# Kernel tuning notes

Measured on AMD Instinct MI355X. Metric: run time of the kernel, lower is better.

Reference implementation:

```python
import jax, jax.numpy as jnp
import numpy as np

N = 262144
C = 256
G = 4096  # number of segments (upper bound on group ids)


def setup_inputs() -> dict:
    key = jax.random.key(0)
    ks = jax.random.split(key, 8)
    s = 1.0 / np.sqrt(C)
    x = jax.random.normal(ks[0], (1, N, C), dtype=jnp.float32)
    ix = jax.random.randint(ks[1], (N,), 0, G, dtype=jnp.int64)
    Wf = jax.random.uniform(ks[2], (C, C), jnp.float32, -s, s)
    bf = jax.random.uniform(ks[3], (C,), jnp.float32, -s, s)
    Wg = jax.random.uniform(ks[4], (C, C), jnp.float32, -s, s)
    bg = jax.random.uniform(ks[5], (C,), jnp.float32, -s, s)
    Wh = jax.random.uniform(ks[6], (C, C), jnp.float32, -s, s)
    bh = jax.random.uniform(ks[7], (C,), jnp.float32, -s, s)
    return {"x": x, "Wf": Wf, "bf": bf, "Wg": Wg, "bg": bg, "Wh": Wh, "bh": bh, "ix": ix}


def reference(x, Wf, bf, Wg, bg, Wh, bh, ix):
    # x: [1, N, C]; only batch 0 is used (matches torch module)
    x0 = x[0]                                    # [N, C]
    fx = x0 @ Wf.T + bf                          # [N, C]
    gx = jnp.clip(x0 @ Wg.T + bg, -50.0, 50.0)   # [N, C]
    exp_gx = jnp.exp(gx)                         # [N, C]
    # Segment softmax: sorting + cumsum group relabel in the torch code is
    # mathematically just a per-group normalized weighted sum keyed by ix.
    seg = ix.astype(jnp.int32)
    denom = jax.ops.segment_sum(exp_gx, seg, num_segments=G)   # [G, C]
    w = exp_gx / denom[seg]                                    # [N, C]
    y = jax.ops.segment_sum(fx * w, seg, num_segments=G)       # [G, C]
    y = y @ Wh.T + bh                                          # [G, C]
    out = y[seg]                                               # [N, C]
    return out[None]                                           # [1, N, C]
```

## Files before the change

### kernel.cpp

```cpp
#include <hip/hip_runtime.h>
#include <stdint.h>
#include <stddef.h>

#define N_ROWS 262144
#define CCH    256
#define NGRP   4096

typedef short bf16x8 __attribute__((ext_vector_type(8)));
typedef short bf16x4 __attribute__((ext_vector_type(4)));
typedef float f32x4  __attribute__((ext_vector_type(4)));

static __device__ __forceinline__ short f2bf(float f){
  union { float f; unsigned u; } v; v.f = f;
  unsigned u = v.u;
  unsigned r = (u + 0x7FFFu + ((u >> 16) & 1u)) >> 16;
  return (short)r;
}

typedef __attribute__((address_space(1))) const unsigned int GU32;
typedef __attribute__((address_space(3))) unsigned int LU32;
static __device__ __forceinline__ void gload_lds16(const void* g, void* l){
  __builtin_amdgcn_global_load_lds((GU32*)g, (LU32*)l, 16, 0, 0);
}

__global__ __launch_bounds__(256) void k_castw(
    const float* __restrict__ Wf, const float* __restrict__ Wg,
    const float* __restrict__ Wh,
    short* __restrict__ wfb, short* __restrict__ wgb, float* __restrict__ wht)
{
  int e = blockIdx.x * 256 + threadIdx.x;
  wfb[e] = f2bf(Wf[e]);
  wgb[e] = f2bf(Wg[e]);
  int k = e >> 8, j = e & 255;
  wht[e] = Wh[j * 256 + k];
}

__global__ __launch_bounds__(256) void k_hist(const int* __restrict__ ix, int* __restrict__ counts){
  int i = blockIdx.x * blockDim.x + threadIdx.x;
  int stride = gridDim.x * blockDim.x;
  for (; i < N_ROWS; i += stride) atomicAdd(&counts[ix[i]], 1);
}

__global__ __launch_bounds__(1024) void k_scan(const int* __restrict__ counts, int* __restrict__ cursor){
  __shared__ int sums[1024];
  int t = threadIdx.x;
  int base = t * 4;
  int c0 = counts[base], c1 = counts[base+1], c2 = counts[base+2], c3 = counts[base+3];
  sums[t] = c0 + c1 + c2 + c3;
  __syncthreads();
  for (int off = 1; off < 1024; off <<= 1){
    int v = (t >= off) ? sums[t - off] : 0;
    __syncthreads();
    sums[t] += v;
    __syncthreads();
  }
  int prev = (t == 0) ? 0 : sums[t - 1];
  cursor[base]   = prev;
  cursor[base+1] = prev + c0;
  cursor[base+2] = prev + c0 + c1;
  cursor[base+3] = prev + c0 + c1 + c2;
}

__global__ __launch_bounds__(256) void k_scatter_cast(
    const int* __restrict__ ix, int* __restrict__ cursor,
    const float* __restrict__ x, short* __restrict__ xb, int* __restrict__ gid)
{
  int wave = threadIdx.x >> 6;
  int lane = threadIdx.x & 63;
  int i = blockIdx.x * 4 + wave;
  int stride = gridDim.x * 4;
  for (; i < N_ROWS; i += stride){
    int g = ix[i];
    int p;
    if (lane == 0) p = atomicAdd(&cursor[g], 1);
    p = __shfl(p, 0);
    f32x4 v = *(const f32x4*)(x + (size_t)i * 256 + lane * 4);
    bf16x4 b;
    #pragma unroll
    for (int j = 0; j < 4; ++j) b[j] = f2bf(v[j]);
    *(bf16x4*)(xb + (size_t)p * 256 + lane * 4) = b;
    if (lane == 0) gid[p] = g;
  }
}

__global__ __launch_bounds__(512, 2) void k_gemm(
    const short* __restrict__ xb,
    const short* __restrict__ wfb, const short* __restrict__ wgb,
    const float* __restrict__ bfp, const float* __restrict__ bgp,
    const int* __restrict__ gid,
    float* __restrict__ numer, float* __restrict__ denom)
{
  __shared__ short bst[64][512];

  const int tid  = threadIdx.x;
  const int wave = tid >> 6;
  const int lane = tid & 63;
  const int l16  = lane & 15;
  const int quad = lane >> 4;

  const int p     = blockIdx.x;
  const int xcd   = p & 7;
  const int ixd   = p >> 3;
  const int cg    = ixd & 3;
  const int bslot = xcd * 16 + (ixd >> 2);
  const int j0    = cg * 64;

  #pragma unroll
  for (int q = 0; q < 8; ++q){
    int f = wave * 8 + q;
    int mat = f >> 5, ks = (f >> 2) & 7, t = f & 3;
    const short* wsrc = mat ? wgb : wfb;
    const short* src = wsrc + (size_t)(j0 + t * 16 + l16) * 256 + ks * 32 + quad * 8;
    gload_lds16(src, &bst[f][0]);
  }
  __syncthreads();

  float bfr[4], bgr[4];
  #pragma unroll
  for (int t = 0; t < 4; ++t){
    bfr[t] = bfp[j0 + t * 16 + l16];
    bgr[t] = bgp[j0 + t * 16 + l16];
  }

  for (int tile = bslot; tile < N_ROWS / 256; tile += 128){
    const int row0 = tile * 256 + wave * 32;
    const int l31  = lane & 31;
    const int gidv = gid[row0 + l31];
    const short* xr0 = xb + (size_t)(row0 + l16) * 256 + quad * 8;
    const short* xr1 = xr0 + 16 * 256;

    f32x4 accF[2][4], accG[2][4];
    #pragma unroll
    for (int rg = 0; rg < 2; ++rg)
      #pragma unroll
      for (int t = 0; t < 4; ++t){
        accF[rg][t] = (f32x4){0.f,0.f,0.f,0.f};
        accG[rg][t] = (f32x4){0.f,0.f,0.f,0.f};
      }

    #pragma unroll
    for (int kc = 0; kc < 4; ++kc){
      bf16x8 a[2][2];
      a[0][0] = *(const bf16x8*)(xr0 + kc * 64);
      a[0][1] = *(const bf16x8*)(xr0 + kc * 64 + 32);
      a[1][0] = *(const bf16x8*)(xr1 + kc * 64);
      a[1][1] = *(const bf16x8*)(xr1 + kc * 64 + 32);
      __builtin_amdgcn_s_setprio(1);
      #pragma unroll
      for (int ks = 0; ks < 2; ++ks){
        const int kk = kc * 2 + ks;
        #pragma unroll
        for (int t = 0; t < 4; ++t){
          bf16x8 bF = *(const bf16x8*)&bst[kk * 4 + t][lane * 8];
          accF[0][t] = __builtin_amdgcn_mfma_f32_16x16x32_bf16(a[0][ks], bF, accF[0][t], 0, 0, 0);
          accF[1][t] = __builtin_amdgcn_mfma_f32_16x16x32_bf16(a[1][ks], bF, accF[1][t], 0, 0, 0);
          bf16x8 bG = *(const bf16x8*)&bst[32 + kk * 4 + t][lane * 8];
          accG[0][t] = __builtin_amdgcn_mfma_f32_16x16x32_bf16(a[0][ks], bG, accG[0][t], 0, 0, 0);
          accG[1][t] = __builtin_amdgcn_mfma_f32_16x16x32_bf16(a[1][ks], bG, accG[1][t], 0, 0, 0);
        }
      }
      __builtin_amdgcn_s_setprio(0);
    }

    #pragma unroll
    for (int rg = 0; rg < 2; ++rg)
      #pragma unroll
      for (int t = 0; t < 4; ++t)
        #pragma unroll
        for (int r = 0; r < 4; ++r){
          float g = accG[rg][t][r] + bgr[t];
          g = fminf(fmaxf(g, -50.f), 50.f);
          float e = __expf(g);
          accF[rg][t][r] = (accF[rg][t][r] + bfr[t]) * e;
          accG[rg][t][r] = e;
        }

    int gprev = __shfl(gidv, (l31 + 31) & 31);
    bool head = (l31 == 0) || (gidv != gprev);
    unsigned long long hb = __ballot(head) & 0xFFFFFFFFull;
    int start = 0;
    while (start < 32){
      int g = __shfl(gidv, start);
      unsigned long long rest = (hb >> 1) >> start;
      int end = rest ? (start + 1 + __builtin_ctzll(rest)) : 32;
      #pragma unroll
      for (int t = 0; t < 4; ++t){
        float sF = 0.f, sE = 0.f;
        #pragma unroll
        for (int rg = 0; rg < 2; ++rg)
          #pragma unroll
          for (int r = 0; r < 4; ++r){
            int rl = rg * 16 + quad * 4 + r;
            bool in = (rl >= start) && (rl < end);
            sF += in ? accF[rg][t][r] : 0.f;
            sE += in ? accG[rg][t][r] : 0.f;
          }
        sF += __shfl_xor(sF, 16); sF += __shfl_xor(sF, 32);
        sE += __shfl_xor(sE, 16); sE += __shfl_xor(sE, 32);
        if (quad == 0){
          atomicAdd(&numer[(size_t)g * 256 + j0 + t * 16 + l16], sF);
          atomicAdd(&denom[(size_t)g * 256 + j0 + t * 16 + l16], sE);
        }
      }
      start = end;
    }
  }
}

__global__ __launch_bounds__(256) void k_yh(
    const float* __restrict__ numer, const float* __restrict__ denom,
    const float* __restrict__ wht, const float* __restrict__ bh,
    float* __restrict__ yh)
{
  __shared__ float ys[16][256];
  int t = threadIdx.x;
  int g0 = blockIdx.x * 16;
  #pragma unroll
  for (int gg = 0; gg < 16; ++gg){
    size_t idx = (size_t)(g0 + gg) * 256 + t;
    float d = denom[idx];
    ys[gg][t] = (d != 0.f) ? (numer[idx] / d) : 0.f;
  }
  __syncthreads();
  float acc[16];
  #pragma unroll
  for (int gg = 0; gg < 16; ++gg) acc[gg] = 0.f;
  for (int k = 0; k < 256; k += 4){
    float w0 = wht[(k+0) * 256 + t];
    float w1 = wht[(k+1) * 256 + t];
    float w2 = wht[(k+2) * 256 + t];
    float w3 = wht[(k+3) * 256 + t];
    #pragma unroll
    for (int gg = 0; gg < 16; ++gg)
      acc[gg] += w0 * ys[gg][k] + w1 * ys[gg][k+1] + w2 * ys[gg][k+2] + w3 * ys[gg][k+3];
  }
  float b = bh[t];
  #pragma unroll
  for (int gg = 0; gg < 16; ++gg) yh[(size_t)(g0 + gg) * 256 + t] = acc[gg] + b;
}

__global__ __launch_bounds__(256) void k_out(const int* __restrict__ ix,
    const float* __restrict__ yh, float* __restrict__ out)
{
  int wave = threadIdx.x >> 6;
  int lane = threadIdx.x & 63;
  int i = blockIdx.x * 4 + wave;
  int stride = gridDim.x * 4;
  for (; i < N_ROWS; i += stride){
    int g = ix[i];
    f32x4 v = *(const f32x4*)(yh + (size_t)g * 256 + lane * 4);
    *(f32x4*)(out + (size_t)i * 256 + lane * 4) = v;
  }
}

extern "C" void kernel_launch(void* const* d_in, const int* in_sizes, int n_in,
                              void* d_out, int out_size, void* d_ws, size_t ws_size,
                              hipStream_t stream)
{
  const float* x  = (const float*)d_in[0];
  const float* Wf = (const float*)d_in[1];
  const float* bf = (const float*)d_in[2];
  const float* Wg = (const float*)d_in[3];
  const float* bg = (const float*)d_in[4];
  const float* Wh = (const float*)d_in[5];
  const float* bh = (const float*)d_in[6];
  const int*   ix = (const int*)d_in[7];
  float* out = (float*)d_out;

  char* ws = (char*)d_ws;
  float* numer  = (float*)(ws + 0);
  float* denom  = (float*)(ws + 4194304);
  int*   counts = (int*)  (ws + 8388608);
  int*   cursor = (int*)  (ws + 8404992);
  float* yh     = (float*)(ws + 8421376);
  float* wht    = (float*)(ws + 12615680);
  short* wfb    = (short*)(ws + 12877824);
  short* wgb    = (short*)(ws + 13008896);
  int*   gid    = (int*)  (ws + 13139968);

  short* xb = (short*)d_out;

  hipMemsetAsync(ws, 0, 8404992, stream);

  k_castw<<<256, 256, 0, stream>>>(Wf, Wg, Wh, wfb, wgb, wht);
  k_hist<<<512, 256, 0, stream>>>(ix, counts);
  k_scan<<<1, 1024, 0, stream>>>(counts, cursor);
  k_scatter_cast<<<2048, 256, 0, stream>>>(ix, cursor, x, xb, gid);
  k_gemm<<<512, 512, 0, stream>>>(xb, wfb, wgb, bf, bg, gid, numer, denom);
  k_yh<<<256, 256, 0, stream>>>(numer, denom, wht, bh, yh);
  k_out<<<2048, 256, 0, stream>>>(ix, yh, out);
}
```

Baseline: 861.2 us.

## Switch gemm to 32x32x16 MFMA with 32-column blocks and more blocks

Rewrites the fused f/g projection kernel to use 32x32x16 bf16 MFMA tiles instead of 16x16x32, so each wave computes 32 rows by 32 output columns per matrix. Blocks shrink to 256 threads covering 32 columns (8 column groups) with half the LDS weight tile, and the grid grows to 2048 blocks. The segment-reduction epilogue is adapted to the 32x32 accumulator layout and needs only one cross-lane shuffle. The intent is fewer MFMA issues and cheaper reductions, but each x row is now reread by 8 column groups instead of 4, which doubles A-operand global traffic.

Result: faster. 794.1 us (-7.8%).

```diff
diff --git a/kernel.cpp b/kernel.cpp
--- a/kernel.cpp
+++ b/kernel.cpp
@@ -9,6 +9,7 @@
 typedef short bf16x8 __attribute__((ext_vector_type(8)));
 typedef short bf16x4 __attribute__((ext_vector_type(4)));
 typedef float f32x4  __attribute__((ext_vector_type(4)));
+typedef float f32x16 __attribute__((ext_vector_type(16)));
 
 static __device__ __forceinline__ short f2bf(float f){
   union { float f; unsigned u; } v; v.f = f;
@@ -83,97 +84,69 @@
   }
 }
 
-__global__ __launch_bounds__(512, 2) void k_gemm(
+__global__ __launch_bounds__(256) void k_gemm(
     const short* __restrict__ xb,
     const short* __restrict__ wfb, const short* __restrict__ wgb,
     const float* __restrict__ bfp, const float* __restrict__ bgp,
     const int* __restrict__ gid,
     float* __restrict__ numer, float* __restrict__ denom)
 {
-  __shared__ short bst[64][512];
+  __shared__ short bst[32][512];
 
   const int tid  = threadIdx.x;
   const int wave = tid >> 6;
   const int lane = tid & 63;
-  const int l16  = lane & 15;
-  const int quad = lane >> 4;
+  const int l31  = lane & 31;
+  const int hi   = lane >> 5;
 
   const int p     = blockIdx.x;
   const int xcd   = p & 7;
   const int ixd   = p >> 3;
-  const int cg    = ixd & 3;
-  const int bslot = xcd * 16 + (ixd >> 2);
-  const int j0    = cg * 64;
+  const int cg    = ixd & 7;
+  const int bslot = xcd * 32 + (ixd >> 3);
+  const int j0    = cg * 32;
 
   #pragma unroll
   for (int q = 0; q < 8; ++q){
     int f = wave * 8 + q;
-    int mat = f >> 5, ks = (f >> 2) & 7, t = f & 3;
+    int mat = f >> 4, ks = f & 15;
     const short* wsrc = mat ? wgb : wfb;
-    const short* src = wsrc + (size_t)(j0 + t * 16 + l16) * 256 + ks * 32 + quad * 8;
+    const short* src = wsrc + (size_t)(j0 + l31) * 256 + ks * 16 + hi * 8;
     gload_lds16(src, &bst[f][0]);
   }
   __syncthreads();
 
-  float bfr[4], bgr[4];
-  #pragma unroll
-  for (int t = 0; t < 4; ++t){
-    bfr[t] = bfp[j0 + t * 16 + l16];
-    bgr[t] = bgp[j0 + t * 16 + l16];
-  }
-
-  for (int tile = bslot; tile < N_ROWS / 256; tile += 128){
-    const int row0 = tile * 256 + wave * 32;
-    const int l31  = lane & 31;
+  const float bfv = bfp[j0 + l31];
+  const float bgv = bgp[j0 + l31];
+
+  for (int tile = bslot; tile < N_ROWS / 128; tile += 256){
+    const int row0 = tile * 128 + wave * 32;
     const int gidv = gid[row0 + l31];
-    const short* xr0 = xb + (size_t)(row0 + l16) * 256 + quad * 8;
-    const short* xr1 = xr0 + 16 * 256;
-
-    f32x4 accF[2][4], accG[2][4];
-    #pragma unroll
-    for (int rg = 0; rg < 2; ++rg)
-      #pragma unroll
-      for (int t = 0; t < 4; ++t){
-        accF[rg][t] = (f32x4){0.f,0.f,0.f,0.f};
-        accG[rg][t] = (f32x4){0.f,0.f,0.f,0.f};
-      }
-
-    #pragma unroll
-    for (int kc = 0; kc < 4; ++kc){
-      bf16x8 a[2][2];
-      a[0][0] = *(const bf16x8*)(xr0 + kc * 64);
-      a[0][1] = *(const bf16x8*)(xr0 + kc * 64 + 32);
-      a[1][0] = *(const bf16x8*)(xr1 + kc * 64);
-      a[1][1] = *(const bf16x8*)(xr1 + kc * 64 + 32);
+    const short* xr = xb + (size_t)(row0 + l31) * 256 + hi * 8;
+
+    f32x16 accF, accG;
+    #pragma unroll
+    for (int r = 0; r < 16; ++r){ accF[r] = 0.f; accG[r] = 0.f; }
+
+    #pragma unroll
+    for (int ks = 0; ks < 16; ++ks){
+      bf16x8 a  = *(const bf16x8*)(xr + ks * 16);
+      bf16x8 bF = *(const bf16x8*)&bst[ks][lane * 8];
+      bf16x8 bG = *(const bf16x8*)&bst[16 + ks][lane * 8];
       __builtin_amdgcn_s_setprio(1);
-      #pragma unroll
-      for (int ks = 0; ks < 2; ++ks){
-        const int kk = kc * 2 + ks;
-        #pragma unroll
-        for (int t = 0; t < 4; ++t){
-          bf16x8 bF = *(const bf16x8*)&bst[kk * 4 + t][lane * 8];
-          accF[0][t] = __builtin_amdgcn_mfma_f32_16x16x32_bf16(a[0][ks], bF, accF[0][t], 0, 0, 0);
-          accF[1][t] = __builtin_amdgcn_mfma_f32_16x16x32_bf16(a[1][ks], bF, accF[1][t], 0, 0, 0);
-          bf16x8 bG = *(const bf16x8*)&bst[32 + kk * 4 + t][lane * 8];
-          accG[0][t] = __builtin_amdgcn_mfma_f32_16x16x32_bf16(a[0][ks], bG, accG[0][t], 0, 0, 0);
-          accG[1][t] = __builtin_amdgcn_mfma_f32_16x16x32_bf16(a[1][ks], bG, accG[1][t], 0, 0, 0);
-        }
-      }
+      accF = __builtin_amdgcn_mfma_f32_32x32x16_bf16(a, bF, accF, 0, 0, 0);
+      accG = __builtin_amdgcn_mfma_f32_32x32x16_bf16(a, bG, accG, 0, 0, 0);
       __builtin_amdgcn_s_setprio(0);
     }
 
     #pragma unroll
-    for (int rg = 0; rg < 2; ++rg)
-      #pragma unroll
-      for (int t = 0; t < 4; ++t)
-        #pragma unroll
-        for (int r = 0; r < 4; ++r){
-          float g = accG[rg][t][r] + bgr[t];
-          g = fminf(fmaxf(g, -50.f), 50.f);
-          float e = __expf(g);
-          accF[rg][t][r] = (accF[rg][t][r] + bfr[t]) * e;
-          accG[rg][t][r] = e;
-        }
+    for (int r = 0; r < 16; ++r){
+      float g = accG[r] + bgv;
+      g = fminf(fmaxf(g, -50.f), 50.f);
+      float e = __expf(g);
+      accF[r] = (accF[r] + bfv) * e;
+      accG[r] = e;
+    }
 
     int gprev = __shfl(gidv, (l31 + 31) & 31);
     bool head = (l31 == 0) || (gidv != gprev);
@@ -181,26 +154,21 @@
     int start = 0;
     while (start < 32){
       int g = __shfl(gidv, start);
-      unsigned long long rest = (hb >> 1) >> start;
+      unsigned long long rest = hb >> (start + 1);
       int end = rest ? (start + 1 + __builtin_ctzll(rest)) : 32;
+      float sF = 0.f, sE = 0.f;
       #pragma unroll
-      for (int t = 0; t < 4; ++t){
-        float sF = 0.f, sE = 0.f;
-        #pragma unroll
-        for (int rg = 0; rg < 2; ++rg)
-          #pragma unroll
-          for (int r = 0; r < 4; ++r){
-            int rl = rg * 16 + quad * 4 + r;
-            bool in = (rl >= start) && (rl < end);
-            sF += in ? accF[rg][t][r] : 0.f;
-            sE += in ? accG[rg][t][r] : 0.f;
-          }
-        sF += __shfl_xor(sF, 16); sF += __shfl_xor(sF, 32);
-        sE += __shfl_xor(sE, 16); sE += __shfl_xor(sE, 32);
-        if (quad == 0){
-          atomicAdd(&numer[(size_t)g * 256 + j0 + t * 16 + l16], sF);
-          atomicAdd(&denom[(size_t)g * 256 + j0 + t * 16 + l16], sE);
-        }
+      for (int r = 0; r < 16; ++r){
+        int row = (r & 3) + 8 * (r >> 2) + 4 * hi;
+        bool in = (row >= start) && (row < end);
+        sF += in ? accF[r] : 0.f;
+        sE += in ? accG[r] : 0.f;
+      }
+      sF += __shfl_xor(sF, 32);
+      sE += __shfl_xor(sE, 32);
+      if (hi == 0){
+        atomicAdd(&numer[(size_t)g * 256 + j0 + l31], sF);
+        atomicAdd(&denom[(size_t)g * 256 + j0 + l31], sE);
       }
       start = end;
     }
@@ -286,7 +254,7 @@
   k_hist<<<512, 256, 0, stream>>>(ix, counts);
   k_scan<<<1, 1024, 0, stream>>>(counts, cursor);
   k_scatter_cast<<<2048, 256, 0, stream>>>(ix, cursor, x, xb, gid);
-  k_gemm<<<512, 512, 0, stream>>>(xb, wfb, wgb, bf, bg, gid, numer, denom);
+  k_gemm<<<2048, 256, 0, stream>>>(xb, wfb, wgb, bf, bg, gid, numer, denom);
   k_yh<<<256, 256, 0, stream>>>(numer, denom, wht, bh, yh);
   k_out<<<2048, 256, 0, stream>>>(ix, yh, out);
 }
```
